# Kernel tuning notes

Hardware: AMD Instinct MI355X
Metric: run time of the kernel (lower is better)

The kernel has to match this reference:

```python
import jax, jax.numpy as jnp
import numpy as np

H = 81  # number_of_cells
EPS = 1e-5

def setup_inputs() -> dict:
    key = jax.random.key(0)
    ks = jax.random.split(key, 16)
    B, T, F = 512, 1024, 128
    s_ih = 1.0 / np.sqrt(H)
    inp = {
        'x':     jax.random.normal(ks[0], (B, 1, T, F), dtype=jnp.float32),
        'W_ih':  jax.random.uniform(ks[1], (3 * H, F), jnp.float32, -s_ih, s_ih),
        'W_hh':  jax.random.uniform(ks[2], (3 * H, H), jnp.float32, -s_ih, s_ih),
        'b_ih':  jax.random.uniform(ks[3], (3 * H,), jnp.float32, -s_ih, s_ih),
        'b_hh':  jax.random.uniform(ks[4], (3 * H,), jnp.float32, -s_ih, s_ih),
        'fc_w':  jax.random.uniform(ks[5], (8, H), jnp.float32, -s_ih, s_ih),
        'fc_b':  jax.random.uniform(ks[6], (8,), jnp.float32, -s_ih, s_ih),
        'g1':    jnp.ones((8,), jnp.float32),
        'beta1': jnp.zeros((8,), jnp.float32),
        'fc1_w': jax.random.uniform(ks[7], (4, 8), jnp.float32, -np.sqrt(1/8), np.sqrt(1/8)),
        'fc1_b': jax.random.uniform(ks[8], (4,), jnp.float32, -np.sqrt(1/8), np.sqrt(1/8)),
        'g2':    jnp.ones((4,), jnp.float32),
        'beta2': jnp.zeros((4,), jnp.float32),
        'fc2_w': jax.random.uniform(ks[9], (1, 4), jnp.float32, -0.5, 0.5),
        'fc2_b': jax.random.uniform(ks[10], (1,), jnp.float32, -0.5, 0.5),
    }
    return inp

def _batchnorm(x, g, b):
    mu = jnp.mean(x, axis=0)
    var = jnp.var(x, axis=0)  # biased, as torch uses for normalization
    return (x - mu) * jax.lax.rsqrt(var + EPS) * g + b

def _gru_last_hidden(x, W_ih, W_hh, b_ih, b_hh):
    # x: [B, T, F]; PyTorch gate order: r, z, n
    B = x.shape[0]
    xg = jnp.einsum('btf,gf->tbg', x, W_ih) + b_ih  # [T, B, 3H]
    h0 = jnp.zeros((B, H), x.dtype)

    def step(h, xg_t):
        hg = h @ W_hh.T + b_hh
        xr, xz, xn = jnp.split(xg_t, 3, axis=-1)
        hr, hz, hn = jnp.split(hg, 3, axis=-1)
        r = jax.nn.sigmoid(xr + hr)
        z = jax.nn.sigmoid(xz + hz)
        n = jnp.tanh(xn + r * hn)
        h_new = (1.0 - z) * n + z * h
        return h_new, None

    h_last, _ = jax.lax.scan(step, h0, xg)
    return h_last  # [B, H]

def reference(x, W_ih, W_hh, b_ih, b_hh, fc_w, fc_b, g1, beta1, fc1_w, fc1_b, g2, beta2, fc2_w, fc2_b):
    B = x.shape[0]
    xs = x.reshape(B, x.shape[2], x.shape[3])  # view(B, T, F)
    h = _gru_last_hidden(xs, W_ih, W_hh, b_ih, b_hh)
    out = h @ fc_w.T + fc_b            # GRU0.fc on last timestep -> [B, 8]
    out = jax.nn.silu(out)
    out = _batchnorm(out, g1, beta1)
    out = jax.nn.silu(out @ fc1_w.T + fc1_b)
    out = _batchnorm(out, g2, beta2)
    out = out @ fc2_w.T + fc2_b        # [B, 1]
    return out
```

## Files before the change

kernel.cpp:

```cpp
#include <hip/hip_runtime.h>

#define B_  512
#define T_  1024
#define F_  128
#define H_  81
#define G3  243
#define GPX 244

typedef unsigned short u16;
typedef __attribute__((ext_vector_type(8))) short bf16x8;
typedef __attribute__((ext_vector_type(4))) float f32x4;
typedef __attribute__((ext_vector_type(2))) float f32x2;

__device__ __forceinline__ float bf2f(u16 u) {
    union { unsigned int i; float f; } v; v.i = ((unsigned int)u) << 16; return v.f;
}
__device__ __forceinline__ u16 f2bf(float f) {
    union { float f; unsigned int i; } v; v.f = f;
    unsigned int i = v.i;
    return (u16)((i + 0x7fffu + ((i >> 16) & 1u)) >> 16);
}
__device__ __forceinline__ float sigmoidf_(float x) { return 1.f / (1.f + __expf(-x)); }
__device__ __forceinline__ float tanhf_(float x) {
    float e = __expf(2.f * x);
    return 1.f - 2.f / (e + 1.f);
}
__device__ __forceinline__ void barrier_nodrain() {
    asm volatile("s_waitcnt lgkmcnt(0)\n\ts_barrier" ::: "memory");
}

__global__ void wsplit_kernel(const float* __restrict__ W,
                              u16* __restrict__ hi, u16* __restrict__ lo)
{
    const int i = blockIdx.x * 256 + threadIdx.x;
    if (i < G3 * F_) {
        const float v = W[i];
        const u16 h = f2bf(v);
        hi[i] = h;
        lo[i] = f2bf(v - bf2f(h));
    }
}

__global__ __launch_bounds__(256, 2) void xg_gemm(const float* __restrict__ x,
                                                  const u16* __restrict__ Whi,
                                                  const u16* __restrict__ Wlo,
                                                  const float* __restrict__ b_ih,
                                                  float* __restrict__ xg)
{
    __shared__ __align__(16) u16 ws_hi[G3][64];
    __shared__ __align__(16) u16 ws_lo[G3][64];

    const int tid  = threadIdx.x;
    const int wave = tid >> 6, lane = tid & 63;
    const int l15  = lane & 15, q = lane >> 4;
    const int b    = blockIdx.x & 511;
    const int t0   = (blockIdx.x >> 9) << 7;

    f32x4 acc[2][16];
#pragma unroll
    for (int mt = 0; mt < 2; ++mt)
#pragma unroll
        for (int gt = 0; gt < 16; ++gt) acc[mt][gt] = (f32x4){0.f, 0.f, 0.f, 0.f};

    for (int half = 0; half < 2; ++half) {
        if (half) __syncthreads();
#pragma unroll
        for (int it = 0; it < 16; ++it) {
            const int i = it * 256 + tid;
            if (i < 2 * G3 * 8) {
                const bool lo = (i >= G3 * 8);
                const int j = lo ? (i - G3 * 8) : i;
                const int g = j >> 3, c = j & 7;
                const uint4 v = *(const uint4*)((lo ? Wlo : Whi)
                                                + (size_t)g * F_ + half * 64 + c * 8);
                *(uint4*)&((lo ? ws_lo : ws_hi)[g][((c + g) & 7) * 8]) = v;
            }
        }
        __syncthreads();

#pragma unroll
        for (int kcl = 0; kcl < 2; ++kcl) {
            bf16x8 aHi[2], aLo[2];
#pragma unroll
            for (int mt = 0; mt < 2; ++mt) {
                const float* xr = x + ((size_t)b * T_ + t0 + (wave * 2 + mt) * 16 + l15) * F_
                                  + half * 64 + kcl * 32 + q * 8;
                float xv[8];
                *(float4*)&xv[0] = *(const float4*)(xr);
                *(float4*)&xv[4] = *(const float4*)(xr + 4);
#pragma unroll
                for (int j = 0; j < 8; ++j) {
                    const u16 h = f2bf(xv[j]);
                    aHi[mt][j] = (short)h;
                    aLo[mt][j] = (short)f2bf(xv[j] - bf2f(h));
                }
            }
#pragma unroll
            for (int gt = 0; gt < 16; ++gt) {
                const int gr  = gt * 16 + l15;
                const int grc = (gr < G3) ? gr : (G3 - 1);
                const int sl  = ((kcl * 4 + q + grc) & 7) * 8;
                const bf16x8 bHi = *(const bf16x8*)&ws_hi[grc][sl];
                const bf16x8 bLo = *(const bf16x8*)&ws_lo[grc][sl];
#pragma unroll
                for (int mt = 0; mt < 2; ++mt) {
                    acc[mt][gt] = __builtin_amdgcn_mfma_f32_16x16x32_bf16(aHi[mt], bHi, acc[mt][gt], 0, 0, 0);
                    acc[mt][gt] = __builtin_amdgcn_mfma_f32_16x16x32_bf16(aHi[mt], bLo, acc[mt][gt], 0, 0, 0);
                    acc[mt][gt] = __builtin_amdgcn_mfma_f32_16x16x32_bf16(aLo[mt], bHi, acc[mt][gt], 0, 0, 0);
                }
            }
        }
    }
#pragma unroll
    for (int gt = 0; gt < 16; ++gt) {
        const int g = gt * 16 + l15;
        if (g < G3) {
            const float bias = b_ih[g];
#pragma unroll
            for (int mt = 0; mt < 2; ++mt) {
                const int trow = t0 + (wave * 2 + mt) * 16 + q * 4;
#pragma unroll
                for (int c = 0; c < 4; ++c)
                    xg[((size_t)b * T_ + trow + c) * GPX + g] = acc[mt][gt][c] + bias;
            }
        }
    }
}

__global__ __launch_bounds__(256, 2) void gru_kernel(const float* __restrict__ xg,
                                                     const float* __restrict__ W_hh,
                                                     const float* __restrict__ b_hh,
                                                     float* __restrict__ h_out)
{
    __shared__ __align__(16) float h_s[84];
    __shared__ float u_s[162];
    __shared__ float xn_s[H_];
    __shared__ float hn_s[H_];

    const int tid = threadIdx.x, b = blockIdx.x;
    const int g = tid;
    const bool active = (g < G3);
    const int grow = active ? g : 0;

    f32x2 w2[42];
    {
        const float* wr = W_hh + (size_t)grow * H_;
#pragma unroll
        for (int j = 0; j < 42; ++j) {
            const float e0 = (active && 2 * j < H_)     ? wr[2 * j]     : 0.f;
            const float e1 = (active && 2 * j + 1 < H_) ? wr[2 * j + 1] : 0.f;
            w2[j] = (f32x2){e0, e1};
        }
    }
    const float bhh = active ? b_hh[grow] : 0.f;

    if (tid < 84) h_s[tid] = 0.f;
    __syncthreads();

    const float* xp = xg + (size_t)b * T_ * GPX + grow;
    float xf[4];
#pragma unroll
    for (int p = 0; p < 4; ++p) xf[p] = xp[(size_t)p * GPX];

    for (int t4 = 0; t4 < T_; t4 += 4) {
#pragma unroll
        for (int u = 0; u < 4; ++u) {
            const float xv = xf[u];
            f32x2 a2 = {bhh, 0.f};
#pragma unroll
            for (int jj = 0; jj < 21; ++jj) {
                const float4 h4 = ((const float4*)h_s)[jj];
                a2 = __builtin_elementwise_fma(w2[2 * jj],     (f32x2){h4.x, h4.y}, a2);
                a2 = __builtin_elementwise_fma(w2[2 * jj + 1], (f32x2){h4.z, h4.w}, a2);
            }
            const float pre = a2.x + a2.y;

            if (g < 162) {
                u_s[g] = xv + pre;
            } else if (g < G3) {
                xn_s[g - 162] = xv;
                hn_s[g - 162] = pre;
            }
            barrier_nodrain();
            if (tid < H_) {
                const float rr = sigmoidf_(u_s[tid]);
                const float zz = sigmoidf_(u_s[H_ + tid]);
                const float nn = tanhf_(fmaf(rr, hn_s[tid], xn_s[tid]));
                h_s[tid] = nn + zz * (h_s[tid] - nn);
            }
            barrier_nodrain();
            const int tn = (t4 + u + 4 < T_) ? (t4 + u + 4) : (T_ - 1);
            xf[u] = xp[(size_t)tn * GPX];
        }
    }

    if (tid < H_) h_out[(size_t)b * H_ + tid] = h_s[tid];
}

__device__ __forceinline__ float block_sum(float v, float* red, int tid) {
#pragma unroll
    for (int off = 32; off; off >>= 1) v += __shfl_down(v, off, 64);
    const int wid = tid >> 6;
    if ((tid & 63) == 0) red[wid] = v;
    __syncthreads();
    if (tid == 0) {
        float s = 0.f;
#pragma unroll
        for (int i = 0; i < 8; ++i) s += red[i];
        red[8] = s;
    }
    __syncthreads();
    const float s = red[8];
    __syncthreads();
    return s;
}

__global__ __launch_bounds__(512) void head_kernel(const float* __restrict__ h_out,
                                                   const float* __restrict__ fc_w,
                                                   const float* __restrict__ fc_b,
                                                   const float* __restrict__ g1,
                                                   const float* __restrict__ beta1,
                                                   const float* __restrict__ fc1_w,
                                                   const float* __restrict__ fc1_b,
                                                   const float* __restrict__ g2,
                                                   const float* __restrict__ beta2,
                                                   const float* __restrict__ fc2_w,
                                                   const float* __restrict__ fc2_b,
                                                   float* __restrict__ out)
{
    __shared__ float red[9];
    const int tid = threadIdx.x;
    const float inv = 1.f / 512.f;

    float hv[H_];
    const float* hp = h_out + (size_t)tid * H_;
#pragma unroll
    for (int c = 0; c < H_; ++c) hv[c] = hp[c];

    float o[8];
#pragma unroll
    for (int j = 0; j < 8; ++j) {
        float s = fc_b[j];
        for (int c = 0; c < H_; ++c) s += hv[c] * fc_w[j * H_ + c];
        o[j] = s * sigmoidf_(s);
    }
#pragma unroll
    for (int j = 0; j < 8; ++j) {
        const float mu = block_sum(o[j], red, tid) * inv;
        const float m2 = block_sum(o[j] * o[j], red, tid) * inv;
        o[j] = (o[j] - mu) * rsqrtf(m2 - mu * mu + 1e-5f) * g1[j] + beta1[j];
    }
    float p[4];
#pragma unroll
    for (int i = 0; i < 4; ++i) {
        float s = fc1_b[i];
#pragma unroll
        for (int j = 0; j < 8; ++j) s += o[j] * fc1_w[i * 8 + j];
        p[i] = s * sigmoidf_(s);
    }
#pragma unroll
    for (int i = 0; i < 4; ++i) {
        const float mu = block_sum(p[i], red, tid) * inv;
        const float m2 = block_sum(p[i] * p[i], red, tid) * inv;
        p[i] = (p[i] - mu) * rsqrtf(m2 - mu * mu + 1e-5f) * g2[i] + beta2[i];
    }
    float res = fc2_b[0];
#pragma unroll
    for (int i = 0; i < 4; ++i) res += p[i] * fc2_w[i];
    out[tid] = res;
}

extern "C" void kernel_launch(void* const* d_in, const int* in_sizes, int n_in,
                              void* d_out, int out_size, void* d_ws, size_t ws_size,
                              hipStream_t stream)
{
    const float* x     = (const float*)d_in[0];
    const float* W_ih  = (const float*)d_in[1];
    const float* W_hh  = (const float*)d_in[2];
    const float* b_ih  = (const float*)d_in[3];
    const float* b_hh  = (const float*)d_in[4];

    float* xg    = (float*)d_ws;
    float* h_out = xg + (size_t)B_ * T_ * GPX;
    u16*   Whi   = (u16*)(h_out + B_ * H_);
    u16*   Wlo   = Whi + G3 * F_;

    wsplit_kernel<<<dim3((G3 * F_ + 255) / 256), dim3(256), 0, stream>>>(W_ih, Whi, Wlo);
    xg_gemm<<<dim3(512 * 8), dim3(256), 0, stream>>>(x, Whi, Wlo, b_ih, xg);
    gru_kernel<<<dim3(B_), dim3(256), 0, stream>>>(xg, W_hh, b_hh, h_out);
    head_kernel<<<dim3(1), dim3(512), 0, stream>>>(h_out,
        (const float*)d_in[5], (const float*)d_in[6], (const float*)d_in[7],
        (const float*)d_in[8], (const float*)d_in[9], (const float*)d_in[10],
        (const float*)d_in[11], (const float*)d_in[12], (const float*)d_in[13],
        (const float*)d_in[14], (float*)d_out);
}
```

Baseline: 1.270 ms.

## Split GRU recurrent matvec along the hidden dimension across three thread groups

Each thread now computes partial dot products for three gates (r, z, n of one hidden unit) over a 28-element slice of h, instead of one full 81-element row. The partial sums go to three shared-memory buffers and are added up by the gate threads. Each thread reads only 7 float4 of h per step instead of 21, which cuts LDS read traffic and shortens the serial FMA chain on the recurrent critical path. In exchange, each step adds extra LDS writes and a three-way reduction. The hidden state is also kept in a register for the update.

```diff
diff --git a/kernel.cpp b/kernel.cpp
--- a/kernel.cpp
+++ b/kernel.cpp
@@ -132,61 +132,92 @@
                                                      const float* __restrict__ b_hh,
                                                      float* __restrict__ h_out)
 {
-    __shared__ __align__(16) float h_s[84];
-    __shared__ float u_s[162];
-    __shared__ float xn_s[H_];
-    __shared__ float hn_s[H_];
+    __shared__ __align__(16) float h_s[88];
+    __shared__ float part0[244];
+    __shared__ float part1[244];
+    __shared__ float part2[244];
+    __shared__ float xn_s[84];
 
     const int tid = threadIdx.x, b = blockIdx.x;
-    const int g = tid;
-    const bool active = (g < G3);
-    const int grow = active ? g : 0;
-
-    f32x2 w2[42];
-    {
-        const float* wr = W_hh + (size_t)grow * H_;
-#pragma unroll
-        for (int j = 0; j < 42; ++j) {
-            const float e0 = (active && 2 * j < H_)     ? wr[2 * j]     : 0.f;
-            const float e1 = (active && 2 * j + 1 < H_) ? wr[2 * j + 1] : 0.f;
-            w2[j] = (f32x2){e0, e1};
-        }
-    }
-    const float bhh = active ? b_hh[grow] : 0.f;
-
-    if (tid < 84) h_s[tid] = 0.f;
+    const bool act = tid < G3;
+    const int p   = (tid >= 162) ? 2 : ((tid >= 81) ? 1 : 0);
+    const int j   = act ? (tid - p * 81) : 0;
+    const int k0  = p * 28;
+
+    f32x2 w2[3][14];
+#pragma unroll
+    for (int i = 0; i < 3; ++i) {
+        const float* wr = W_hh + (size_t)(j + 81 * i) * H_ + k0;
+#pragma unroll
+        for (int c = 0; c < 14; ++c) {
+            const float e0 = (act && (k0 + 2 * c)     < H_) ? wr[2 * c]     : 0.f;
+            const float e1 = (act && (k0 + 2 * c + 1) < H_) ? wr[2 * c + 1] : 0.f;
+            w2[i][c] = (f32x2){e0, e1};
+        }
+    }
+#pragma unroll
+    for (int i = 0; i < 3; ++i)
+#pragma unroll
+        for (int c = 0; c < 14; ++c)
+            asm volatile("" : "+v"(w2[i][c]));
+
+    const bool gth = tid < H_;
+    const float br = gth ? b_hh[tid]          : 0.f;
+    const float bz = gth ? b_hh[H_ + tid]     : 0.f;
+    const float bn = gth ? b_hh[2 * H_ + tid] : 0.f;
+    float hreg = 0.f;
+
+    if (tid < 88) h_s[tid] = 0.f;
     __syncthreads();
 
-    const float* xp = xg + (size_t)b * T_ * GPX + grow;
+    float* const pp = (p == 0) ? part0 : ((p == 1) ? part1 : part2);
+
+    const float* xp = xg + (size_t)b * T_ * GPX + (act ? tid : 0);
     float xf[4];
 #pragma unroll
-    for (int p = 0; p < 4; ++p) xf[p] = xp[(size_t)p * GPX];
+    for (int u = 0; u < 4; ++u) xf[u] = xp[(size_t)u * GPX];
 
     for (int t4 = 0; t4 < T_; t4 += 4) {
 #pragma unroll
         for (int u = 0; u < 4; ++u) {
             const float xv = xf[u];
-            f32x2 a2 = {bhh, 0.f};
-#pragma unroll
-            for (int jj = 0; jj < 21; ++jj) {
-                const float4 h4 = ((const float4*)h_s)[jj];
-                a2 = __builtin_elementwise_fma(w2[2 * jj],     (f32x2){h4.x, h4.y}, a2);
-                a2 = __builtin_elementwise_fma(w2[2 * jj + 1], (f32x2){h4.z, h4.w}, a2);
-            }
-            const float pre = a2.x + a2.y;
-
-            if (g < 162) {
-                u_s[g] = xv + pre;
-            } else if (g < G3) {
-                xn_s[g - 162] = xv;
-                hn_s[g - 162] = pre;
+            f32x2 aA[3], aB[3];
+#pragma unroll
+            for (int i = 0; i < 3; ++i) { aA[i] = (f32x2){0.f, 0.f}; aB[i] = (f32x2){0.f, 0.f}; }
+#pragma unroll
+            for (int c = 0; c < 7; ++c) {
+                const float4 h4 = ((const float4*)h_s)[p * 7 + c];
+                const f32x2 hlo = {h4.x, h4.y}, hhi = {h4.z, h4.w};
+#pragma unroll
+                for (int i = 0; i < 3; ++i) {
+                    aA[i] = __builtin_elementwise_fma(w2[i][2 * c],     hlo, aA[i]);
+                    aB[i] = __builtin_elementwise_fma(w2[i][2 * c + 1], hhi, aB[i]);
+                }
+            }
+            const f32x2 t0v = aA[0] + aB[0];
+            const f32x2 t1v = aA[1] + aB[1];
+            const f32x2 t2v = aA[2] + aB[2];
+            float s0 = t0v.x + t0v.y;
+            float s1 = t1v.x + t1v.y;
+            float s2 = t2v.x + t2v.y;
+            s0 += (p == 0) ? xv : 0.f;
+            s1 += (p == 1) ? xv : 0.f;
+            if (act) {
+                if (p == 2) xn_s[j] = xv;
+                pp[j]       = s0;
+                pp[j + 81]  = s1;
+                pp[j + 162] = s2;
             }
             barrier_nodrain();
-            if (tid < H_) {
-                const float rr = sigmoidf_(u_s[tid]);
-                const float zz = sigmoidf_(u_s[H_ + tid]);
-                const float nn = tanhf_(fmaf(rr, hn_s[tid], xn_s[tid]));
-                h_s[tid] = nn + zz * (h_s[tid] - nn);
+            if (gth) {
+                const float prer = part0[tid]       + part1[tid]       + part2[tid]       + br;
+                const float prez = part0[tid + 81]  + part1[tid + 81]  + part2[tid + 81]  + bz;
+                const float hn   = part0[tid + 162] + part1[tid + 162] + part2[tid + 162] + bn;
+                const float rr = sigmoidf_(prer);
+                const float zz = sigmoidf_(prez);
+                const float nn = tanhf_(fmaf(rr, hn, xn_s[tid]));
+                hreg = nn + zz * (hreg - nn);
+                h_s[tid] = hreg;
             }
             barrier_nodrain();
             const int tn = (t4 + u + 4 < T_) ? (t4 + u + 4) : (T_ - 1);
@@ -194,7 +225,7 @@
         }
     }
 
-    if (tid < H_) h_out[(size_t)b * H_ + tid] = h_s[tid];
+    if (gth) h_out[(size_t)b * H_ + tid] = hreg;
 }
 
 __device__ __forceinline__ float block_sum(float v, float* red, int tid) {
```

Measured after the change: 1.150 ms. 9.5% less time.

## Restructure GRU recurrence so each thread owns one hidden unit's three gates

Applied to the files above, without the earlier changes.

The GRU kernel now runs 128 threads per batch row. Each active thread holds the r, z and n weight rows in registers and computes all three gate dot products, then applies the nonlinearities itself. Hidden state is double-buffered in shared memory, which cuts each timestep to a single barrier and removes the gate staging arrays. Sigmoid and tanh also switch to hardware reciprocal. The trade-off is about 252 weight registers per thread and three times the serial FMA work per thread, with only two waves per block and fewer threads to hide latency.

```diff
diff --git a/kernel.cpp b/kernel.cpp
--- a/kernel.cpp
+++ b/kernel.cpp
@@ -20,10 +20,10 @@
     unsigned int i = v.i;
     return (u16)((i + 0x7fffu + ((i >> 16) & 1u)) >> 16);
 }
-__device__ __forceinline__ float sigmoidf_(float x) { return 1.f / (1.f + __expf(-x)); }
+__device__ __forceinline__ float rcp_(float x) { return __builtin_amdgcn_rcpf(x); }
+__device__ __forceinline__ float sigmoidf_(float x) { return rcp_(1.f + __expf(-x)); }
 __device__ __forceinline__ float tanhf_(float x) {
-    float e = __expf(2.f * x);
-    return 1.f - 2.f / (e + 1.f);
+    return fmaf(-2.f, rcp_(__expf(2.f * x) + 1.f), 1.f);
 }
 __device__ __forceinline__ void barrier_nodrain() {
     asm volatile("s_waitcnt lgkmcnt(0)\n\ts_barrier" ::: "memory");
@@ -127,74 +127,90 @@
     }
 }
 
-__global__ __launch_bounds__(256, 2) void gru_kernel(const float* __restrict__ xg,
+__global__ __launch_bounds__(128, 1) void gru_kernel(const float* __restrict__ xg,
                                                      const float* __restrict__ W_hh,
                                                      const float* __restrict__ b_hh,
                                                      float* __restrict__ h_out)
 {
-    __shared__ __align__(16) float h_s[84];
-    __shared__ float u_s[162];
-    __shared__ float xn_s[H_];
-    __shared__ float hn_s[H_];
+    __shared__ __align__(16) float h_s[2][88];
 
     const int tid = threadIdx.x, b = blockIdx.x;
-    const int g = tid;
-    const bool active = (g < G3);
-    const int grow = active ? g : 0;
-
-    f32x2 w2[42];
-    {
-        const float* wr = W_hh + (size_t)grow * H_;
-#pragma unroll
-        for (int j = 0; j < 42; ++j) {
-            const float e0 = (active && 2 * j < H_)     ? wr[2 * j]     : 0.f;
-            const float e1 = (active && 2 * j + 1 < H_) ? wr[2 * j + 1] : 0.f;
-            w2[j] = (f32x2){e0, e1};
-        }
-    }
-    const float bhh = active ? b_hh[grow] : 0.f;
-
-    if (tid < 84) h_s[tid] = 0.f;
+    const bool act = tid < H_;
+    const int g = act ? tid : 0;
+
+    f32x2 w2[3][42];
+#pragma unroll
+    for (int i = 0; i < 3; ++i) {
+        const float* wr = W_hh + (size_t)(g + 81 * i) * H_;
+#pragma unroll
+        for (int c = 0; c < 42; ++c) {
+            const float e0 = (act && 2 * c     < H_) ? wr[2 * c]     : 0.f;
+            const float e1 = (act && 2 * c + 1 < H_) ? wr[2 * c + 1] : 0.f;
+            w2[i][c] = (f32x2){e0, e1};
+        }
+    }
+#pragma unroll
+    for (int i = 0; i < 3; ++i)
+#pragma unroll
+        for (int c = 0; c < 42; ++c)
+            asm volatile("" : "+v"(w2[i][c]));
+
+    const float br = act ? b_hh[g]          : 0.f;
+    const float bz = act ? b_hh[H_ + g]     : 0.f;
+    const float bn = act ? b_hh[2 * H_ + g] : 0.f;
+    float hreg = 0.f;
+
+    if (tid < 176) ((float*)h_s)[tid] = 0.f;
     __syncthreads();
 
-    const float* xp = xg + (size_t)b * T_ * GPX + grow;
-    float xf[4];
-#pragma unroll
-    for (int p = 0; p < 4; ++p) xf[p] = xp[(size_t)p * GPX];
-
+    const float* xp = xg + (size_t)b * T_ * GPX + g;
+    float xr[4], xz[4], xn[4];
+#pragma unroll
+    for (int u = 0; u < 4; ++u) {
+        xr[u] = xp[(size_t)u * GPX];
+        xz[u] = xp[(size_t)u * GPX + 81];
+        xn[u] = xp[(size_t)u * GPX + 162];
+    }
+
+    int cur = 0;
     for (int t4 = 0; t4 < T_; t4 += 4) {
 #pragma unroll
         for (int u = 0; u < 4; ++u) {
-            const float xv = xf[u];
-            f32x2 a2 = {bhh, 0.f};
-#pragma unroll
-            for (int jj = 0; jj < 21; ++jj) {
-                const float4 h4 = ((const float4*)h_s)[jj];
-                a2 = __builtin_elementwise_fma(w2[2 * jj],     (f32x2){h4.x, h4.y}, a2);
-                a2 = __builtin_elementwise_fma(w2[2 * jj + 1], (f32x2){h4.z, h4.w}, a2);
-            }
-            const float pre = a2.x + a2.y;
-
-            if (g < 162) {
-                u_s[g] = xv + pre;
-            } else if (g < G3) {
-                xn_s[g - 162] = xv;
-                hn_s[g - 162] = pre;
-            }
+            const int t = t4 + u;
+            f32x2 a0A = {0.f, 0.f}, a0B = {0.f, 0.f};
+            f32x2 a1A = {0.f, 0.f}, a1B = {0.f, 0.f};
+            f32x2 a2A = {0.f, 0.f}, a2B = {0.f, 0.f};
+            const float4* hb = (const float4*)h_s[cur & 1];
+#pragma unroll
+            for (int c = 0; c < 21; ++c) {
+                const float4 h4 = hb[c];
+                const f32x2 lo = {h4.x, h4.y}, hi = {h4.z, h4.w};
+                a0A = __builtin_elementwise_fma(w2[0][2 * c],     lo, a0A);
+                a0B = __builtin_elementwise_fma(w2[0][2 * c + 1], hi, a0B);
+                a1A = __builtin_elementwise_fma(w2[1][2 * c],     lo, a1A);
+                a1B = __builtin_elementwise_fma(w2[1][2 * c + 1], hi, a1B);
+                a2A = __builtin_elementwise_fma(w2[2][2 * c],     lo, a2A);
+                a2B = __builtin_elementwise_fma(w2[2][2 * c + 1], hi, a2B);
+            }
+            const f32x2 t0 = a0A + a0B, t1 = a1A + a1B, t2 = a2A + a2B;
+            const float hr = t0.x + t0.y + br;
+            const float hz = t1.x + t1.y + bz;
+            const float hn = t2.x + t2.y + bn;
+            const float rr = sigmoidf_(xr[u] + hr);
+            const float zz = sigmoidf_(xz[u] + hz);
+            const float nn = tanhf_(fmaf(rr, hn, xn[u]));
+            hreg = nn + zz * (hreg - nn);
+            if (act) h_s[(cur & 1) ^ 1][g] = hreg;
             barrier_nodrain();
-            if (tid < H_) {
-                const float rr = sigmoidf_(u_s[tid]);
-                const float zz = sigmoidf_(u_s[H_ + tid]);
-                const float nn = tanhf_(fmaf(rr, hn_s[tid], xn_s[tid]));
-                h_s[tid] = nn + zz * (h_s[tid] - nn);
-            }
-            barrier_nodrain();
-            const int tn = (t4 + u + 4 < T_) ? (t4 + u + 4) : (T_ - 1);
-            xf[u] = xp[(size_t)tn * GPX];
-        }
-    }
-
-    if (tid < H_) h_out[(size_t)b * H_ + tid] = h_s[tid];
+            cur ^= 1;
+            const int tn = (t + 4 < T_) ? (t + 4) : (T_ - 1);
+            xr[u] = xp[(size_t)tn * GPX];
+            xz[u] = xp[(size_t)tn * GPX + 81];
+            xn[u] = xp[(size_t)tn * GPX + 162];
+        }
+    }
+
+    if (act) h_out[(size_t)b * H_ + g] = hreg;
 }
 
 __device__ __forceinline__ float block_sum(float v, float* red, int tid) {
@@ -287,7 +303,7 @@
 
     wsplit_kernel<<<dim3((G3 * F_ + 255) / 256), dim3(256), 0, stream>>>(W_ih, Whi, Wlo);
     xg_gemm<<<dim3(512 * 8), dim3(256), 0, stream>>>(x, Whi, Wlo, b_ih, xg);
-    gru_kernel<<<dim3(B_), dim3(256), 0, stream>>>(xg, W_hh, b_hh, h_out);
+    gru_kernel<<<dim3(B_), dim3(128), 0, stream>>>(xg, W_hh, b_hh, h_out);
     head_kernel<<<dim3(1), dim3(512), 0, stream>>>(h_out,
         (const float*)d_in[5], (const float*)d_in[6], (const float*)d_in[7],
         (const float*)d_in[8], (const float*)d_in[9], (const float*)d_in[10],
```

Result: slower. 1.543 ms (+21.4%).
